# Kernel optimization log

Hardware: AMD Instinct MI355X
Metric: run time of the kernel (lower is better)

The kernel has to match this reference:

```python
import jax, jax.numpy as jnp
import numpy as np
from jax import lax

KH = KW = 3
K = KH * KW
STRIDE = 1
PAD = 1
DIL = 1
GN_GROUPS = 32
EPS = 1e-5


def setup_inputs() -> dict:
    key = jax.random.key(0)
    k0, k1, k2 = jax.random.split(key, 3)
    B, C, H, W = 8, 256, 64, 64
    O = 256
    x = jax.random.normal(k0, (B, C, H, W), jnp.float32)
    # offset-predicting conv (DeformConv2dPack.conv_offset); small weights keep offsets ~O(1)
    w_off = jax.random.normal(k1, (2 * K, C, KH, KW), jnp.float32) * 0.01
    b_off = jnp.zeros((2 * K,), jnp.float32)
    w_dcn = jax.random.normal(k2, (O, C, KH, KW), jnp.float32) * (1.0 / np.sqrt(C * K))
    gamma = jnp.ones((O,), jnp.float32)
    beta = jnp.zeros((O,), jnp.float32)
    return {"x": x, "w_off": w_off, "b_off": b_off, "w_dcn": w_dcn, "gamma": gamma, "beta": beta}


def _deform_conv(x, w_off, b_off, w_dcn):
    B, C, H, W = x.shape
    O = w_dcn.shape[0]
    # offsets via standard conv: [B, 2K, Ho, Wo]; channel layout (k, (dy, dx))
    offset = lax.conv_general_dilated(
        x, w_off, (STRIDE, STRIDE), [(PAD, PAD), (PAD, PAD)],
        rhs_dilation=(DIL, DIL), dimension_numbers=("NCHW", "OIHW", "NCHW"))
    offset = offset + b_off[None, :, None, None]
    Ho, Wo = offset.shape[2], offset.shape[3]
    off = offset.reshape(B, K, 2, Ho, Wo)
    ky = jnp.repeat(jnp.arange(KH), KW)  # [K]
    kx = jnp.tile(jnp.arange(KW), KH)    # [K]
    base_y = (jnp.arange(Ho) * STRIDE - PAD)[None, :, None] + (ky * DIL)[:, None, None]  # [K,Ho,1]
    base_x = (jnp.arange(Wo) * STRIDE - PAD)[None, None, :] + (kx * DIL)[:, None, None]  # [K,1,Wo]
    py = off[:, :, 0] + base_y[None].astype(off.dtype)  # [B,K,Ho,Wo]
    px = off[:, :, 1] + base_x[None].astype(off.dtype)

    def sample_one(xi, py_i, px_i):  # xi [C,H,W]; py/px [K,Ho,Wo]
        y0 = jnp.floor(py_i)
        x0 = jnp.floor(px_i)
        dy = py_i - y0
        dx = px_i - x0
        y0i = y0.astype(jnp.int32)
        x0i = x0.astype(jnp.int32)

        def gather(yi, xj, w):
            valid = (yi >= 0) & (yi < H) & (xj >= 0) & (xj < W)
            yc = jnp.clip(yi, 0, H - 1)
            xc = jnp.clip(xj, 0, W - 1)
            return xi[:, yc, xc] * (w * valid)[None]  # [C,K,Ho,Wo]

        return (gather(y0i, x0i, (1 - dy) * (1 - dx))
                + gather(y0i, x0i + 1, (1 - dy) * dx)
                + gather(y0i + 1, x0i, dy * (1 - dx))
                + gather(y0i + 1, x0i + 1, dy * dx))

    cols = jax.vmap(sample_one)(x, py, px)  # [B,C,K,Ho,Wo]
    y = jnp.einsum("ock,bckp->bop", w_dcn.reshape(O, C, K),
                   cols.reshape(B, C, K, Ho * Wo))
    return y.reshape(B, O, Ho, Wo)


def _group_norm(y, gamma, beta):
    B, O, Ho, Wo = y.shape
    g = y.reshape(B, GN_GROUPS, O // GN_GROUPS, Ho, Wo)
    mean = g.mean(axis=(2, 3, 4), keepdims=True)
    var = g.var(axis=(2, 3, 4), keepdims=True)
    yn = ((g - mean) * lax.rsqrt(var + EPS)).reshape(B, O, Ho, Wo)
    return yn * gamma[None, :, None, None] + beta[None, :, None, None]


def reference(x, w_off, b_off, w_dcn, gamma, beta):
    y = _deform_conv(x, w_off, b_off, w_dcn)
    y = _group_norm(y, gamma, beta)
    return y * jnp.tanh(jax.nn.softplus(y))  # Mish
```

## Files before the change

### kernel.cpp

```cpp
#include <hip/hip_runtime.h>
#include <hip/hip_bf16.h>
#include <math.h>

typedef __bf16 bf16x8 __attribute__((ext_vector_type(8)));
typedef float f32x4 __attribute__((ext_vector_type(4)));
typedef unsigned int u32;
typedef u32 u32x4 __attribute__((ext_vector_type(4)));
typedef u32 u32x2 __attribute__((ext_vector_type(2)));


__device__ inline u32 pack2bf16(float a, float b) {
  u32 ua = __float_as_uint(a);
  u32 ub = __float_as_uint(b);
  ua += 0x7fffu + ((ua >> 16) & 1u);
  ub += 0x7fffu + ((ub >> 16) & 1u);
  return (ua >> 16) | (ub & 0xffff0000u);
}

__global__ void prep(const float* __restrict__ w_dcn, const float* __restrict__ w_off,
                     unsigned short* __restrict__ wT4, unsigned short* __restrict__ wOffT,
                     float* __restrict__ stats) {
  size_t id = (size_t)blockIdx.x * 256 + threadIdx.x;
  if (id < 589824) {
    int o  = (int)(id / 2304);
    int ck = (int)(id % 2304);
    int k = ck >> 8, c = ck & 255;
    float v = w_dcn[(size_t)(o * 256 + c) * 9 + k];
    u32 uv = __float_as_uint(v);
    uv += 0x7fffu + ((uv >> 16) & 1u);
    int tile = ck >> 6, kk = ck & 63;
    int lin = o * 128 + kk * 2;
    int swz = lin ^ ((o & 7) << 4);
    *(unsigned short*)((char*)wT4 + (size_t)tile * 32768 + swz) = (unsigned short)(uv >> 16);
  } else if (id < 663552) {
    int r = (int)(id - 589824);
    int tile = r >> 11;
    int rr = r & 2047;
    int o = rr >> 6, kk = rr & 63;
    int k = tile >> 2, cc = tile & 3;
    int c = (cc << 6) + kk;
    float v = (o < 18) ? w_off[(size_t)(o * 256 + c) * 9 + k] : 0.f;
    u32 uv = __float_as_uint(v);
    uv += 0x7fffu + ((uv >> 16) & 1u);
    int swz = (o * 128 + kk * 2) ^ ((o & 7) << 4);
    *(unsigned short*)((char*)wOffT + (size_t)tile * 4096 + swz) = (unsigned short)(uv >> 16);
  } else if (id < 664064) {
    stats[id - 663552] = 0.f;
  }
}

__global__ __launch_bounds__(256) void transpose_x(const float* __restrict__ x,
                                                   unsigned short* __restrict__ xT) {
  __shared__ float tl[64][65];
  int bx = blockIdx.x;
  int b = bx >> 8;
  int y = (bx >> 2) & 63;
  int cb = (bx & 3) << 6;
  int t = threadIdx.x;
  int xi = t & 63, cr = t >> 6;
  size_t base = (((size_t)(b * 256 + cb) * 64 + y) << 6);
#pragma unroll
  for (int rep = 0; rep < 16; ++rep) {
    int cl = rep * 4 + cr;
    tl[cl][xi] = x[base + (size_t)cl * 4096 + xi];
  }
  __syncthreads();
  int xw = t >> 2, c4 = (t & 3) << 4;
  unsigned short* dst = xT + (((size_t)b * 4096) + y * 64 + xw) * 256 + cb + c4;
  u32 pk[8];
#pragma unroll
  for (int e = 0; e < 8; ++e)
    pk[e] = pack2bf16(tl[c4 + 2 * e][xw], tl[c4 + 2 * e + 1][xw]);
  u32x4 v0 = {pk[0], pk[1], pk[2], pk[3]};
  u32x4 v1 = {pk[4], pk[5], pk[6], pk[7]};
  *(u32x4*)dst = v0;
  *((u32x4*)dst + 1) = v1;
}

__global__ __launch_bounds__(256, 2) void conv_offset_mfma(
    const unsigned short* __restrict__ xT, const unsigned short* __restrict__ wOffT,
    float* __restrict__ offs) {
  __shared__ unsigned short A[2][64][64];
  __shared__ unsigned short Bo[2][2048];
  const int bx = blockIdx.x;
  const int lb = ((bx & 7) << 6) + (bx >> 3);
  const int b = lb >> 6;
  const int y = lb & 63;
  const int t = threadIdx.x;
  const int lane = t & 63, wid = t >> 6;
  const unsigned short* xTb = xT + ((size_t)b << 20);
  const int p = t >> 2;
  const int q16 = (t & 3) << 4;

  f32x4 acc[2];
  {
    f32x4 z = {0.f, 0.f, 0.f, 0.f};
    acc[0] = z; acc[1] = z;
  }

  u32x4 ra = {0u,0u,0u,0u}, rb = {0u,0u,0u,0u};

  auto issue = [&](int tt, int d) {
    int k = tt >> 2, cc = tt & 3;
    int ky = k / 3, kx = k - ky * 3;
    int ys = y - 1 + ky;
    int xs = p - 1 + kx;
    bool ok = ((unsigned)ys < 64u) && ((unsigned)xs < 64u);
    u32x4 z = {0u,0u,0u,0u};
    ra = z; rb = z;
    if (ok) {
      const unsigned short* s0 = xTb + (size_t)(((ys << 6) + xs) << 8) + (cc << 6) + q16;
      ra = *(const u32x4*)s0;
      rb = *(const u32x4*)(s0 + 8);
    }
    __builtin_amdgcn_global_load_lds(
        (const __attribute__((address_space(1))) u32*)((const char*)wOffT + ((size_t)tt << 12) + (wid << 10) + (lane << 4)),
        (__attribute__((address_space(3))) u32*)((char*)&Bo[d][0] + (wid << 10)),
        16, 0, 0);
  };
  auto writeA = [&](int d) {
    char* dst = (char*)&A[d][0][0] + p * 128;
    int b0 = (t & 3) << 5;
    int sw = (p & 7) << 4;
    *(u32x4*)(dst + (b0 ^ sw)) = ra;
    *(u32x4*)(dst + ((b0 + 16) ^ sw)) = rb;
  };

  issue(0, 0);
  writeA(0);
  __syncthreads();

  int cur = 0;
  for (int tt = 0; tt < 36; ++tt) {
    if (tt < 35) issue(tt + 1, cur ^ 1);
#pragma unroll
    for (int s = 0; s < 2; ++s) {
      int row = (wid << 4) + (lane & 15);
      int bir = ((s << 6) + ((lane >> 4) << 4)) ^ ((row & 7) << 4);
      bf16x8 a = *(const bf16x8*)((const char*)&A[cur][0][0] + row * 128 + bir);
#pragma unroll
      for (int j = 0; j < 2; ++j) {
        int o = (j << 4) + (lane & 15);
        int kb = ((s << 6) + ((lane >> 4) << 4)) ^ ((o & 7) << 4);
        bf16x8 bv = *(const bf16x8*)((const char*)&Bo[cur][0] + o * 128 + kb);
        acc[j] = __builtin_amdgcn_mfma_f32_16x16x32_bf16(a, bv, acc[j], 0, 0, 0);
      }
    }
    if (tt < 35) writeA(cur ^ 1);
    __syncthreads();
    cur ^= 1;
  }

#pragma unroll
  for (int j = 0; j < 2; ++j) {
    int o = (j << 4) + (lane & 15);
    if (o < 18) {
#pragma unroll
      for (int r = 0; r < 4; ++r) {
        int pl = (wid << 4) + ((lane >> 4) << 2) + r;
        offs[((size_t)b * 4096 + (y << 6) + pl) * 18 + o] = acc[j][r];
      }
    }
  }
}

union Arena {
  struct {
    unsigned short A[2][128][64];
    unsigned short Bt[2][16384];
  } m;
  unsigned short ytile[256][136];
};

__global__ __launch_bounds__(512, 2) void dcn_main(
    const unsigned short* __restrict__ xT, const float* __restrict__ offs,
    const float* __restrict__ boff, const unsigned short* __restrict__ wT4,
    unsigned short* __restrict__ yb, float* __restrict__ stats) {
  __shared__ Arena ar;
  __shared__ unsigned short poffu[128][9][4];
  __shared__ float pw[128][9][4];

  const int bx = blockIdx.x;
  const int lb = ((bx & 7) << 5) + (bx >> 3);
  const int b = lb >> 5;
  const int pxbase = (lb & 31) << 7;
  const int t = threadIdx.x;
  const int lane = t & 63, wid = t >> 6;
  const bool is_cons = (wid < 4);
  const int obase = (wid & 3) << 6;
  const unsigned short* xTb = xT + ((size_t)b << 20);

  const int q = ((wid & 3) << 6) + lane;
  const int p_my = q >> 1;
  const int half = q & 1;

  for (int idx = t; idx < 1152; idx += 512) {
    int p = idx / 9, k = idx - p * 9;
    int pxg = pxbase + p;
    int yy = pxg >> 6, xx = pxg & 63;
    const float* op = offs + ((size_t)b * 4096 + pxg) * 18 + k * 2;
    int kyi = k / 3, kxi = k - kyi * 3;
    float py = op[0] + boff[k * 2] + (float)(yy - 1 + kyi);
    float pxf = op[1] + boff[k * 2 + 1] + (float)(xx - 1 + kxi);
    float fy = floorf(py), fx = floorf(pxf);
    float dy = py - fy, dx = pxf - fx;
    int y0 = (int)fy, x0 = (int)fx;
    int y1 = y0 + 1, x1 = x0 + 1;
    float vy0 = ((unsigned)y0 < 64u) ? 1.f : 0.f;
    float vy1 = ((unsigned)y1 < 64u) ? 1.f : 0.f;
    float vx0 = ((unsigned)x0 < 64u) ? 1.f : 0.f;
    float vx1 = ((unsigned)x1 < 64u) ? 1.f : 0.f;
    int y0c = min(max(y0, 0), 63), y1c = min(max(y1, 0), 63);
    int x0c = min(max(x0, 0), 63), x1c = min(max(x1, 0), 63);
    poffu[p][k][0] = (unsigned short)((y0c << 6) + x0c);
    poffu[p][k][1] = (unsigned short)((y0c << 6) + x1c);
    poffu[p][k][2] = (unsigned short)((y1c << 6) + x0c);
    poffu[p][k][3] = (unsigned short)((y1c << 6) + x1c);
    pw[p][k][0] = (1.f - dy) * (1.f - dx) * vy0 * vx0;
    pw[p][k][1] = (1.f - dy) * dx * vy0 * vx1;
    pw[p][k][2] = dy * (1.f - dx) * vy1 * vx0;
    pw[p][k][3] = dy * dx * vy1 * vx1;
  }

  f32x4 acc[8][4];
#pragma unroll
  for (int i = 0; i < 8; ++i)
#pragma unroll
    for (int j = 0; j < 4; ++j) {
      f32x4 z = {0.f, 0.f, 0.f, 0.f};
      acc[i][j] = z;
    }

  __syncthreads();

  auto stage = [&](int nt, int d) {
    int k = nt >> 2, cc = nt & 3;
    int cb = (cc << 6) + (half << 5);
    const unsigned short* s0 = xTb + ((int)poffu[p_my][k][0] << 8) + cb;
    const unsigned short* s1 = xTb + ((int)poffu[p_my][k][1] << 8) + cb;
    const unsigned short* s2 = xTb + ((int)poffu[p_my][k][2] << 8) + cb;
    const unsigned short* s3 = xTb + ((int)poffu[p_my][k][3] << 8) + cb;
    u32x4 r0[4], r1[4], r2[4], r3[4];
#pragma unroll
    for (int v = 0; v < 4; ++v) {
      r0[v] = *(const u32x4*)(s0 + (v << 3));
      r1[v] = *(const u32x4*)(s1 + (v << 3));
      r2[v] = *(const u32x4*)(s2 + (v << 3));
      r3[v] = *(const u32x4*)(s3 + (v << 3));
    }
    {
      const char* src = (const char*)wT4 + ((size_t)nt << 15) + ((wid & 3) << 13);
      char* dstb = (char*)&ar.m.Bt[d][0] + ((wid & 3) << 13);
#pragma unroll
      for (int i2 = 0; i2 < 8; ++i2) {
        __builtin_amdgcn_global_load_lds(
            (const __attribute__((address_space(1))) u32*)(src + (i2 << 10) + (lane << 4)),
            (__attribute__((address_space(3))) u32*)(dstb + (i2 << 10)),
            16, 0, 0);
      }
    }
    float w0 = pw[p_my][k][0], w1 = pw[p_my][k][1];
    float w2 = pw[p_my][k][2], w3 = pw[p_my][k][3];
    char* dst = (char*)&ar.m.A[d][0][0] + p_my * 128;
    int sw = (p_my & 7) << 4;
#pragma unroll
    for (int v = 0; v < 4; ++v) {
      u32 o4[4];
#pragma unroll
      for (int e = 0; e < 4; ++e) {
        u32 u0 = r0[v][e], u1 = r1[v][e], u2 = r2[v][e], u3 = r3[v][e];
        float lo = w0 * __uint_as_float(u0 << 16);
        lo = fmaf(w1, __uint_as_float(u1 << 16), lo);
        lo = fmaf(w2, __uint_as_float(u2 << 16), lo);
        lo = fmaf(w3, __uint_as_float(u3 << 16), lo);
        float hi = w0 * __uint_as_float(u0 & 0xffff0000u);
        hi = fmaf(w1, __uint_as_float(u1 & 0xffff0000u), hi);
        hi = fmaf(w2, __uint_as_float(u2 & 0xffff0000u), hi);
        hi = fmaf(w3, __uint_as_float(u3 & 0xffff0000u), hi);
        u32 r;
        asm("v_cvt_pk_bf16_f32 %0, %1, %2" : "=v"(r) : "v"(lo), "v"(hi));
        o4[e] = r;
      }
      u32x4 ov = {o4[0], o4[1], o4[2], o4[3]};
      *(u32x4*)(dst + (((half << 6) + (v << 4)) ^ sw)) = ov;
    }
  };

  if (!is_cons) stage(0, 0);
  __syncthreads();

  int cur = 0;
  for (int tt = 0; tt < 36; ++tt) {
    if (is_cons) {
      const char* Abase = (const char*)&ar.m.A[cur][0][0];
      const char* Bbase = (const char*)&ar.m.Bt[cur][0];
      __builtin_amdgcn_s_setprio(1);
#pragma unroll
      for (int s = 0; s < 2; ++s) {
        int kx = (s << 6) + ((lane >> 4) << 4);
        int swl = (lane & 7) << 4;
        bf16x8 a[8], bb[4];
#pragma unroll
        for (int i = 0; i < 8; ++i)
          a[i] = *(const bf16x8*)(Abase + ((i << 4) + (lane & 15)) * 128 + (kx ^ swl));
#pragma unroll
        for (int j = 0; j < 4; ++j)
          bb[j] = *(const bf16x8*)(Bbase + (obase + (j << 4) + (lane & 15)) * 128 + (kx ^ swl));
#pragma unroll
        for (int i = 0; i < 8; ++i)
#pragma unroll
          for (int j = 0; j < 4; ++j)
            acc[i][j] = __builtin_amdgcn_mfma_f32_16x16x32_bf16(a[i], bb[j], acc[i][j], 0, 0, 0);
      }
      __builtin_amdgcn_s_setprio(0);
    } else {
      if (tt < 35) stage(tt + 1, cur ^ 1);
    }
    __syncthreads();
    cur ^= 1;
  }

  if (is_cons) {
#pragma unroll
    for (int j = 0; j < 4; ++j) {
      float s1 = 0.f, s2 = 0.f;
#pragma unroll
      for (int i = 0; i < 8; ++i)
#pragma unroll
        for (int r = 0; r < 4; ++r) {
          float v = acc[i][j][r];
          s1 += v;
          s2 += v * v;
        }
      s1 += __shfl_xor(s1, 1, 64);  s2 += __shfl_xor(s2, 1, 64);
      s1 += __shfl_xor(s1, 2, 64);  s2 += __shfl_xor(s2, 2, 64);
      s1 += __shfl_xor(s1, 4, 64);  s2 += __shfl_xor(s2, 4, 64);
      s1 += __shfl_xor(s1, 16, 64); s2 += __shfl_xor(s2, 16, 64);
      s1 += __shfl_xor(s1, 32, 64); s2 += __shfl_xor(s2, 32, 64);
      if ((lane & 0x37) == 0) {
        int g = (obase + (j << 4) + (lane & 15)) >> 3;
        atomicAdd(&stats[((b << 5) + g) * 2 + 0], s1);
        atomicAdd(&stats[((b << 5) + g) * 2 + 1], s2);
      }
    }
#pragma unroll
    for (int i = 0; i < 8; ++i)
#pragma unroll
      for (int j = 0; j < 4; ++j) {
        int o = obase + (j << 4) + (lane & 15);
        int pxr = (i << 4) + ((lane >> 4) << 2);
        u32 w0, w1;
        asm("v_cvt_pk_bf16_f32 %0, %1, %2" : "=v"(w0) : "v"(acc[i][j][0]), "v"(acc[i][j][1]));
        asm("v_cvt_pk_bf16_f32 %0, %1, %2" : "=v"(w1) : "v"(acc[i][j][2]), "v"(acc[i][j][3]));
        u32x2 wv = {w0, w1};
        *(u32x2*)((char*)ar.ytile + o * 272 + pxr * 2) = wv;
      }
  }
  __syncthreads();
  {
    int o = t >> 1, hf = t & 1;
    const char* srcb = (const char*)ar.ytile + o * 272 + (hf << 7);
    unsigned short* dst = yb + (((size_t)(b * 256 + o)) << 12) + pxbase + (hf << 6);
#pragma unroll
    for (int qq = 0; qq < 8; ++qq)
      *(u32x4*)((char*)dst + (qq << 4)) = *(const u32x4*)(srcb + (qq << 4));
  }
}

__global__ __launch_bounds__(256) void gn_mish(const unsigned short* __restrict__ yb,
                                               const float* __restrict__ stats,
                                               const float* __restrict__ gamma,
                                               const float* __restrict__ beta,
                                               float* __restrict__ out) {
  int v = blockIdx.x * 512 + threadIdx.x;
#pragma unroll
  for (int it = 0; it < 2; ++it, v += 256) {
    int o = (v >> 9) & 255;
    int b = v >> 17;
    float s1 = stats[((b << 5) + (o >> 3)) * 2 + 0];
    float s2 = stats[((b << 5) + (o >> 3)) * 2 + 1];
    float mean = s1 * (1.f / 32768.f);
    float var = s2 * (1.f / 32768.f) - mean * mean;
    float rstd = rsqrtf(var + 1e-5f);
    float ga = gamma[o] * rstd, be = beta[o] - mean * gamma[o] * rstd;
    u32x4 u = *(const u32x4*)(yb + ((size_t)v << 3));
    float res[8];
#pragma unroll
    for (int e = 0; e < 4; ++e) {
      float va = __uint_as_float(u[e] << 16);
      float vb = __uint_as_float(u[e] & 0xffff0000u);
      float v0 = fmaf(va, ga, be);
      float v1 = fmaf(vb, ga, be);
      float e0 = expf(fminf(v0, 15.f));
      float e1 = expf(fminf(v1, 15.f));
      float n0 = e0 * (e0 + 2.f);
      float n1 = e1 * (e1 + 2.f);
      float m0 = v0 * (n0 / (n0 + 2.f));
      float m1 = v1 * (n1 / (n1 + 2.f));
      if (v0 > 15.f) m0 = v0;
      if (v1 > 15.f) m1 = v1;
      res[2 * e] = m0;
      res[2 * e + 1] = m1;
    }
    f32x4 o0 = {res[0], res[1], res[2], res[3]};
    f32x4 o1 = {res[4], res[5], res[6], res[7]};
    float* dst = out + ((size_t)v << 3);
    *(f32x4*)dst = o0;
    *((f32x4*)dst + 1) = o1;
  }
}

extern "C" void kernel_launch(void* const* d_in, const int* in_sizes, int n_in,
                              void* d_out, int out_size, void* d_ws, size_t ws_size,
                              hipStream_t stream) {
  const float* x     = (const float*)d_in[0];
  const float* w_off = (const float*)d_in[1];
  const float* b_off = (const float*)d_in[2];
  const float* w_dcn = (const float*)d_in[3];
  const float* gamma = (const float*)d_in[4];
  const float* beta  = (const float*)d_in[5];
  float* out = (float*)d_out;
  char* ws = (char*)d_ws;
  unsigned short* xT   = (unsigned short*)(ws);
  unsigned short* yb   = (unsigned short*)(ws + 16777216);
  float* offs          = (float*)(ws + 33554432);
  unsigned short* wT4  = (unsigned short*)(ws + 35913728);
  unsigned short* wOffT= (unsigned short*)(ws + 37093376);
  float* stats         = (float*)(ws + 37240832);
  prep<<<dim3(2594), dim3(256), 0, stream>>>(w_dcn, w_off, wT4, wOffT, stats);
  transpose_x<<<dim3(2048), dim3(256), 0, stream>>>(x, xT);
  conv_offset_mfma<<<dim3(512), dim3(256), 0, stream>>>(xT, wOffT, offs);
  dcn_main<<<dim3(256), dim3(512), 0, stream>>>(xT, offs, b_off, wT4, yb, stats);
  gn_mish<<<dim3(2048), dim3(256), 0, stream>>>(yb, stats, gamma, beta, out);
}
```

Baseline: 134.0 us.

## Store bf16 input in channel-group-major layout for coalesced deformable gathers

The transposed bf16 input moves from pixel-major with 256 channels contiguous to a layout with 8-channel groups outermost, so each 16-byte vector holds 8 channels of one pixel. Producer threads are remapped so consecutive lanes handle consecutive pixels for the same channel group, and the per-pixel offset and weight tables become k-major. The goal is to make the bilinear-sample gather loads from neighbouring lanes hit nearby addresses instead of 512-byte strided rows, and to avoid LDS bank conflicts when reading the tables. The conv_offset kernel is updated to read the new layout. Its two loads per thread now sit 64 KB apart, which may hurt its coalescing.

```diff
diff --git a/kernel.cpp b/kernel.cpp
--- a/kernel.cpp
+++ b/kernel.cpp
@@ -65,16 +65,18 @@
     tl[cl][xi] = x[base + (size_t)cl * 4096 + xi];
   }
   __syncthreads();
-  int xw = t >> 2, c4 = (t & 3) << 4;
-  unsigned short* dst = xT + (((size_t)b * 4096) + y * 64 + xw) * 256 + cb + c4;
-  u32 pk[8];
-#pragma unroll
-  for (int e = 0; e < 8; ++e)
-    pk[e] = pack2bf16(tl[c4 + 2 * e][xw], tl[c4 + 2 * e + 1][xw]);
-  u32x4 v0 = {pk[0], pk[1], pk[2], pk[3]};
-  u32x4 v1 = {pk[4], pk[5], pk[6], pk[7]};
-  *(u32x4*)dst = v0;
-  *((u32x4*)dst + 1) = v1;
+  int xw = t & 63, cpair = t >> 6;
+#pragma unroll
+  for (int r = 0; r < 2; ++r) {
+    int cgl = cpair * 2 + r;
+    int cg = (cb >> 3) + cgl;
+    u32 pk4[4];
+#pragma unroll
+    for (int i = 0; i < 4; ++i)
+      pk4[i] = pack2bf16(tl[cgl * 8 + 2 * i][xw], tl[cgl * 8 + 2 * i + 1][xw]);
+    u32x4 v = {pk4[0], pk4[1], pk4[2], pk4[3]};
+    *(u32x4*)((char*)xT + (((size_t)b << 21)) + ((size_t)cg << 16) + ((y << 6) + xw) * 16) = v;
+  }
 }
 
 __global__ __launch_bounds__(256, 2) void conv_offset_mfma(
@@ -88,9 +90,8 @@
   const int y = lb & 63;
   const int t = threadIdx.x;
   const int lane = t & 63, wid = t >> 6;
-  const unsigned short* xTb = xT + ((size_t)b << 20);
+  const char* xTbB = (const char*)xT + ((size_t)b << 21);
   const int p = t >> 2;
-  const int q16 = (t & 3) << 4;
 
   f32x4 acc[2];
   {
@@ -109,9 +110,10 @@
     u32x4 z = {0u,0u,0u,0u};
     ra = z; rb = z;
     if (ok) {
-      const unsigned short* s0 = xTb + (size_t)(((ys << 6) + xs) << 8) + (cc << 6) + q16;
+      int cg0 = (cc << 3) + ((t & 3) << 1);
+      const char* s0 = xTbB + ((size_t)cg0 << 16) + (((ys << 6) + xs) << 4);
       ra = *(const u32x4*)s0;
-      rb = *(const u32x4*)(s0 + 8);
+      rb = *(const u32x4*)(s0 + 65536);
     }
     __builtin_amdgcn_global_load_lds(
         (const __attribute__((address_space(1))) u32*)((const char*)wOffT + ((size_t)tt << 12) + (wid << 10) + (lane << 4)),
@@ -177,8 +179,8 @@
     const float* __restrict__ boff, const unsigned short* __restrict__ wT4,
     unsigned short* __restrict__ yb, float* __restrict__ stats) {
   __shared__ Arena ar;
-  __shared__ unsigned short poffu[128][9][4];
-  __shared__ float pw[128][9][4];
+  __shared__ unsigned short poffu[9][128][4];
+  __shared__ float pw[9][128][4];
 
   const int bx = blockIdx.x;
   const int lb = ((bx & 7) << 5) + (bx >> 3);
@@ -188,11 +190,11 @@
   const int lane = t & 63, wid = t >> 6;
   const bool is_cons = (wid < 4);
   const int obase = (wid & 3) << 6;
-  const unsigned short* xTb = xT + ((size_t)b << 20);
-
-  const int q = ((wid & 3) << 6) + lane;
-  const int p_my = q >> 1;
-  const int half = q & 1;
+  const char* xTbB = (const char*)xT + ((size_t)b << 21);
+
+  const int pwid = wid - 4;
+  const int p_my = ((pwid & 1) << 6) + lane;
+  const int chalf = pwid >> 1;
 
   for (int idx = t; idx < 1152; idx += 512) {
     int p = idx / 9, k = idx - p * 9;
@@ -212,14 +214,14 @@
     float vx1 = ((unsigned)x1 < 64u) ? 1.f : 0.f;
     int y0c = min(max(y0, 0), 63), y1c = min(max(y1, 0), 63);
     int x0c = min(max(x0, 0), 63), x1c = min(max(x1, 0), 63);
-    poffu[p][k][0] = (unsigned short)((y0c << 6) + x0c);
-    poffu[p][k][1] = (unsigned short)((y0c << 6) + x1c);
-    poffu[p][k][2] = (unsigned short)((y1c << 6) + x0c);
-    poffu[p][k][3] = (unsigned short)((y1c << 6) + x1c);
-    pw[p][k][0] = (1.f - dy) * (1.f - dx) * vy0 * vx0;
-    pw[p][k][1] = (1.f - dy) * dx * vy0 * vx1;
-    pw[p][k][2] = dy * (1.f - dx) * vy1 * vx0;
-    pw[p][k][3] = dy * dx * vy1 * vx1;
+    poffu[k][p][0] = (unsigned short)((y0c << 6) + x0c);
+    poffu[k][p][1] = (unsigned short)((y0c << 6) + x1c);
+    poffu[k][p][2] = (unsigned short)((y1c << 6) + x0c);
+    poffu[k][p][3] = (unsigned short)((y1c << 6) + x1c);
+    pw[k][p][0] = (1.f - dy) * (1.f - dx) * vy0 * vx0;
+    pw[k][p][1] = (1.f - dy) * dx * vy0 * vx1;
+    pw[k][p][2] = dy * (1.f - dx) * vy1 * vx0;
+    pw[k][p][3] = dy * dx * vy1 * vx1;
   }
 
   f32x4 acc[8][4];
@@ -235,22 +237,23 @@
 
   auto stage = [&](int nt, int d) {
     int k = nt >> 2, cc = nt & 3;
-    int cb = (cc << 6) + (half << 5);
-    const unsigned short* s0 = xTb + ((int)poffu[p_my][k][0] << 8) + cb;
-    const unsigned short* s1 = xTb + ((int)poffu[p_my][k][1] << 8) + cb;
-    const unsigned short* s2 = xTb + ((int)poffu[p_my][k][2] << 8) + cb;
-    const unsigned short* s3 = xTb + ((int)poffu[p_my][k][3] << 8) + cb;
+    int cgb = (cc << 3) + (chalf << 2);
+    const char* s0 = xTbB + ((int)poffu[k][p_my][0] << 4);
+    const char* s1 = xTbB + ((int)poffu[k][p_my][1] << 4);
+    const char* s2 = xTbB + ((int)poffu[k][p_my][2] << 4);
+    const char* s3 = xTbB + ((int)poffu[k][p_my][3] << 4);
     u32x4 r0[4], r1[4], r2[4], r3[4];
 #pragma unroll
     for (int v = 0; v < 4; ++v) {
-      r0[v] = *(const u32x4*)(s0 + (v << 3));
-      r1[v] = *(const u32x4*)(s1 + (v << 3));
-      r2[v] = *(const u32x4*)(s2 + (v << 3));
-      r3[v] = *(const u32x4*)(s3 + (v << 3));
+      size_t po = ((size_t)(cgb + v) << 16);
+      r0[v] = *(const u32x4*)(s0 + po);
+      r1[v] = *(const u32x4*)(s1 + po);
+      r2[v] = *(const u32x4*)(s2 + po);
+      r3[v] = *(const u32x4*)(s3 + po);
     }
     {
-      const char* src = (const char*)wT4 + ((size_t)nt << 15) + ((wid & 3) << 13);
-      char* dstb = (char*)&ar.m.Bt[d][0] + ((wid & 3) << 13);
+      const char* src = (const char*)wT4 + ((size_t)nt << 15) + (pwid << 13);
+      char* dstb = (char*)&ar.m.Bt[d][0] + (pwid << 13);
 #pragma unroll
       for (int i2 = 0; i2 < 8; ++i2) {
         __builtin_amdgcn_global_load_lds(
@@ -259,8 +262,8 @@
             16, 0, 0);
       }
     }
-    float w0 = pw[p_my][k][0], w1 = pw[p_my][k][1];
-    float w2 = pw[p_my][k][2], w3 = pw[p_my][k][3];
+    float w0 = pw[k][p_my][0], w1 = pw[k][p_my][1];
+    float w2 = pw[k][p_my][2], w3 = pw[k][p_my][3];
     char* dst = (char*)&ar.m.A[d][0][0] + p_my * 128;
     int sw = (p_my & 7) << 4;
 #pragma unroll
@@ -282,7 +285,7 @@
         o4[e] = r;
       }
       u32x4 ov = {o4[0], o4[1], o4[2], o4[3]};
-      *(u32x4*)(dst + (((half << 6) + (v << 4)) ^ sw)) = ov;
+      *(u32x4*)(dst + (((chalf << 6) + (v << 4)) ^ sw)) = ov;
     }
   };
 
```

After: 135.3 us. About the same (+0.9%).
